# Kernel optimization log

Measured on AMD Instinct MI355X. Metric: run time of the kernel, lower is better.

The kernel has to match this reference:

```python
import jax, jax.numpy as jnp
import numpy as np

N = 50000        # nodes
E = 800000       # edges
IN_C = 128       # in_channels
HID = 256        # hidden_channels
HEADS = 4
HD = HID // HEADS
LAYERS = 4
GRAPHS = 64
OUT_C = 32
MAX_POS = 10
EPS = 1e-5


def layer_norm(x, g, b):
    mu = jnp.mean(x, axis=-1, keepdims=True)
    var = jnp.mean((x - mu) ** 2, axis=-1, keepdims=True)
    return (x - mu) / jnp.sqrt(var + EPS) * g + b


def setup_inputs() -> dict:
    key = jax.random.key(0)
    ks = jax.random.split(key, 32)
    s = 0.02
    inp = {
        "x": jax.random.normal(ks[0], (N, IN_C), dtype=jnp.float32),
        "edge_index": jax.random.randint(ks[1], (2, E), 0, N, dtype=jnp.int32),
        "pos_idx": jax.random.randint(ks[2], (N,), 0, MAX_POS, dtype=jnp.int32),
        "batch": jnp.sort(jax.random.randint(ks[3], (N,), 0, GRAPHS, dtype=jnp.int32)),
        # encoder MLP: Linear(IN->HID), ReLU, LN(HID), Linear(HID->HID); weights stored [in,out]
        "enc_w1": jax.random.normal(ks[4], (IN_C, HID)) * s,
        "enc_b1": jnp.zeros((HID,), jnp.float32),
        "enc_g": jnp.ones((HID,), jnp.float32),
        "enc_beta": jnp.zeros((HID,), jnp.float32),
        "enc_w2": jax.random.normal(ks[5], (HID, HID)) * s,
        "enc_b2": jnp.zeros((HID,), jnp.float32),
        "pos_emb": jax.random.normal(ks[6], (MAX_POS, HID)) * s,
        # stacked attention-layer params [LAYERS, ...]
        "Wq": jax.random.normal(ks[7], (LAYERS, HID, HID)) * s,
        "bq": jnp.zeros((LAYERS, HID), jnp.float32),
        "Wk": jax.random.normal(ks[8], (LAYERS, HID, HID)) * s,
        "bk": jnp.zeros((LAYERS, HID), jnp.float32),
        "Wv": jax.random.normal(ks[9], (LAYERS, HID, HID)) * s,
        "bv": jnp.zeros((LAYERS, HID), jnp.float32),
        "mlp_w1": jax.random.normal(ks[10], (LAYERS, 2 * HID, HID)) * s,
        "mlp_b1": jnp.zeros((LAYERS, HID), jnp.float32),
        "mlp_g": jnp.ones((LAYERS, HID), jnp.float32),
        "mlp_beta": jnp.zeros((LAYERS, HID), jnp.float32),
        "mlp_w2": jax.random.normal(ks[11], (LAYERS, HID, HID)) * s,
        "mlp_b2": jnp.zeros((LAYERS, HID), jnp.float32),
        # classifier
        "cls_w1": jax.random.normal(ks[12], (HID, HID)) * s,
        "cls_b1": jnp.zeros((HID,), jnp.float32),
        "cls_g": jnp.ones((HID,), jnp.float32),
        "cls_beta": jnp.zeros((HID,), jnp.float32),
        "cls_w2": jax.random.normal(ks[13], (HID, OUT_C)) * s,
        "cls_b2": jnp.zeros((OUT_C,), jnp.float32),
    }
    return inp


def reference(x, edge_index, pos_idx, batch,
              enc_w1, enc_b1, enc_g, enc_beta, enc_w2, enc_b2, pos_emb,
              Wq, bq, Wk, bk, Wv, bv,
              mlp_w1, mlp_b1, mlp_g, mlp_beta, mlp_w2, mlp_b2,
              cls_w1, cls_b1, cls_g, cls_beta, cls_w2, cls_b2):
    row, col = edge_index[0], edge_index[1]
    n = x.shape[0]
    e = row.shape[0]

    # NodeEncoder
    h = layer_norm(jax.nn.relu(x @ enc_w1 + enc_b1), enc_g, enc_beta) @ enc_w2 + enc_b2
    h = h + pos_emb[pos_idx]

    scale = jnp.asarray(HD, h.dtype) ** 0.5
    for l in range(LAYERS):
        Q = (h @ Wq[l] + bq[l]).reshape(n, HEADS, HD)
        K = (h @ Wk[l] + bk[l]).reshape(n, HEADS, HD)
        V = (h @ Wv[l] + bv[l]).reshape(n, HEADS, HD)
        # per-edge attention scores [E, HEADS]
        scores = jnp.sum(Q[row] * K[col], axis=-1) / scale
        # segment softmax over destination node `row`
        m = jax.ops.segment_max(scores, row, num_segments=n)
        ex = jnp.exp(scores - m[row])
        denom = jax.ops.segment_sum(ex, row, num_segments=n)
        w = ex / denom[row]                         # [E, HEADS]
        msg = (w[..., None] * V[col]).reshape(e, HID)
        agg = jax.ops.segment_sum(msg, row, num_segments=n)  # [N, HID]
        cat = jnp.concatenate([h, agg], axis=-1)
        z = layer_norm(jax.nn.relu(cat @ mlp_w1[l] + mlp_b1[l]), mlp_g[l], mlp_beta[l]) @ mlp_w2[l] + mlp_b2[l]
        h = z + h

    # global mean pool over graphs
    sums = jax.ops.segment_sum(h, batch, num_segments=GRAPHS)
    cnt = jax.ops.segment_sum(jnp.ones((n, 1), h.dtype), batch, num_segments=GRAPHS)
    pooled = sums / jnp.maximum(cnt, 1.0)

    out = layer_norm(jax.nn.relu(pooled @ cls_w1 + cls_b1), cls_g, cls_beta) @ cls_w2 + cls_b2
    return out
```

## Files before the change

kernel.cpp:

```cpp
#include <hip/hip_runtime.h>
#include <cstdint>

#define HID 256
#define HEADS 4
#define GRAPHS 64
#define OUTC 32
#define EPSV 1e-5f
#define PSPLIT 32

typedef __bf16 b16x8 __attribute__((ext_vector_type(8)));
typedef float  f32x4 __attribute__((ext_vector_type(4)));

__device__ __forceinline__ f32x4 mfma16(b16x8 a, b16x8 b, f32x4 c) {
    return __builtin_amdgcn_mfma_f32_16x16x32_bf16(a, b, c, 0, 0, 0);
}

__device__ __forceinline__ unsigned int pack_bf16(float a, float b) {
    unsigned short ua = __builtin_bit_cast(unsigned short, (__bf16)a);
    unsigned short ub = __builtin_bit_cast(unsigned short, (__bf16)b);
    return (unsigned int)ua | ((unsigned int)ub << 16);
}

__device__ __forceinline__ void unpack2(unsigned int u, float& lo, float& hi) {
    lo = __builtin_bit_cast(float, u << 16);
    hi = __builtin_bit_cast(float, u & 0xffff0000u);
}

__device__ __forceinline__ float b2f(unsigned short u) {
    return __builtin_bit_cast(float, (unsigned int)u << 16);
}

__device__ __forceinline__ void stage_gld128(char* buf, const unsigned short* __restrict__ src,
                                             int base, int tid)
{
#pragma unroll
    for (int i = 0; i < 16; i++) {
        int idx = i * 256 + tid;
        int r = idx >> 5;
        int u = idx & 31;
        int us = u ^ (r & 7);
        const void* gp = (const void*)(src + (size_t)(base + r) * HID + us * 8);
        __builtin_amdgcn_global_load_lds(
            (const __attribute__((address_space(1))) void*)gp,
            (__attribute__((address_space(3))) void*)(buf + idx * 16),
            16, 0, 0);
    }
}

__global__ __launch_bounds__(256) void wtrans_kernel(const float* __restrict__ W,
    unsigned short* __restrict__ Wt, int K, int C)
{
    __shared__ float tile[32][33];
    const float* Wm = W + (size_t)blockIdx.z * K * C;
    unsigned short* Wtm = Wt + (size_t)blockIdx.z * K * C;
    int k0 = blockIdx.x * 32, c0 = blockIdx.y * 32;
    int tx = threadIdx.x & 31, ty = threadIdx.x >> 5;
#pragma unroll
    for (int i = 0; i < 32; i += 8)
        tile[ty + i][tx] = Wm[(size_t)(k0 + ty + i) * C + c0 + tx];
    __syncthreads();
#pragma unroll
    for (int i = 0; i < 32; i += 8) {
        float v = tile[tx][ty + i];
        Wtm[(size_t)(c0 + ty + i) * K + k0 + tx] =
            __builtin_bit_cast(unsigned short, (__bf16)v);
    }
}

__global__ __launch_bounds__(256) void enc1_mfma(
    const float* __restrict__ in0, const unsigned short* __restrict__ Wt,
    const float* __restrict__ bias, const float* __restrict__ g,
    const float* __restrict__ be, unsigned short* __restrict__ outb, int n)
{
    constexpr int KTILE = 128, ROWB = 256;
    __shared__ __align__(16) char alds[64 * 256];
    __shared__ float red[4][64][2];
    int tid = threadIdx.x, lane = tid & 63, wv = tid >> 6;
    int cg = lane & 15, rg = lane >> 4;
    int base = blockIdx.x * 64;
    int cbase = wv * 64;

    f32x4 acc[4][4];
#pragma unroll
    for (int m = 0; m < 4; m++)
#pragma unroll
        for (int f = 0; f < 4; f++) acc[m][f] = (f32x4){0.f, 0.f, 0.f, 0.f};

#pragma unroll
    for (int i = 0; i < 8; i++) {
        int idx = (i * 256 + tid) * 4;
        int row = idx >> 7, k = idx & 127;
        int node = base + row;
        float4 v = {0.f, 0.f, 0.f, 0.f};
        if (node < n) v = *(const float4*)(in0 + (size_t)node * KTILE + k);
        uint2 pp; pp.x = pack_bf16(v.x, v.y); pp.y = pack_bf16(v.z, v.w);
        int off = row * ROWB + k * 2;
        off ^= (row & 7) << 4;
        *(uint2*)(alds + off) = pp;
    }
    __syncthreads();

#pragma unroll 2
    for (int k0 = 0; k0 < KTILE; k0 += 32) {
        b16x8 a[4], b[4];
#pragma unroll
        for (int m = 0; m < 4; m++) {
            int R = m * 16 + cg;
            int off = R * ROWB + (k0 + rg * 8) * 2;
            off ^= (R & 7) << 4;
            a[m] = __builtin_bit_cast(b16x8, *(const uint4*)(alds + off));
        }
#pragma unroll
        for (int f = 0; f < 4; f++) {
            const unsigned short* p = Wt + (size_t)(cbase + f * 16 + cg) * KTILE + k0 + rg * 8;
            b[f] = __builtin_bit_cast(b16x8, *(const uint4*)p);
        }
#pragma unroll
        for (int m = 0; m < 4; m++)
#pragma unroll
            for (int f = 0; f < 4; f++)
                acc[m][f] = mfma16(a[m], b[f], acc[m][f]);
    }

    float bias_v[4], g_v[4], be_v[4];
#pragma unroll
    for (int f = 0; f < 4; f++) {
        int col = cbase + f * 16 + cg;
        bias_v[f] = bias[col]; g_v[f] = g[col]; be_v[f] = be[col];
    }
#pragma unroll
    for (int m = 0; m < 4; m++)
#pragma unroll
        for (int f = 0; f < 4; f++)
#pragma unroll
            for (int r = 0; r < 4; r++)
                acc[m][f][r] = fmaxf(acc[m][f][r] + bias_v[f], 0.f);
#pragma unroll
    for (int m = 0; m < 4; m++)
#pragma unroll
        for (int r = 0; r < 4; r++) {
            float s = acc[m][0][r] + acc[m][1][r] + acc[m][2][r] + acc[m][3][r];
            float q = acc[m][0][r] * acc[m][0][r] + acc[m][1][r] * acc[m][1][r]
                    + acc[m][2][r] * acc[m][2][r] + acc[m][3][r] * acc[m][3][r];
#pragma unroll
            for (int o = 1; o < 16; o <<= 1) {
                s += __shfl_xor(s, o, 64); q += __shfl_xor(q, o, 64);
            }
            if (cg == 0) { int R = m * 16 + rg * 4 + r; red[wv][R][0] = s; red[wv][R][1] = q; }
        }
    __syncthreads();
#pragma unroll
    for (int m = 0; m < 4; m++)
#pragma unroll
        for (int r = 0; r < 4; r++) {
            int R = m * 16 + rg * 4 + r;
            float S = red[0][R][0] + red[1][R][0] + red[2][R][0] + red[3][R][0];
            float Q = red[0][R][1] + red[1][R][1] + red[2][R][1] + red[3][R][1];
            float mu = S * (1.f / HID);
            float rs = rsqrtf(Q * (1.f / HID) - mu * mu + EPSV);
            int row = base + R;
            if (row >= n) continue;
            size_t ro = (size_t)row * HID;
#pragma unroll
            for (int f = 0; f < 4; f++) {
                float v = (acc[m][f][r] - mu) * rs * g_v[f] + be_v[f];
                outb[ro + cbase + f * 16 + cg] = __builtin_bit_cast(unsigned short, (__bf16)v);
            }
        }
}

template<int NPASS, bool RELU_LN, bool ADD_RES, bool POS>
__global__ __launch_bounds__(256) void gemm128(
    const unsigned short* __restrict__ in0, const unsigned short* __restrict__ in1,
    const unsigned short* __restrict__ Wt, const float* __restrict__ bias,
    const float* __restrict__ g, const float* __restrict__ be,
    const unsigned short* __restrict__ addsrc, const float* __restrict__ pos_emb,
    const int* __restrict__ pidx, unsigned short* __restrict__ outb, int n)
{
    constexpr int KS = 256 * NPASS;
    __shared__ __align__(16) char alds[128 * 512];
    __shared__ float red[4][128][2];

    int tid = threadIdx.x, lane = tid & 63, wv = tid >> 6;
    int cg = lane & 15, rg = lane >> 4;
    int base = blockIdx.x * 128;
    int cbase = wv * 64;

    f32x4 acc[2][4][4];
#pragma unroll
    for (int t = 0; t < 2; t++)
#pragma unroll
        for (int m = 0; m < 4; m++)
#pragma unroll
            for (int f = 0; f < 4; f++) acc[t][m][f] = (f32x4){0.f, 0.f, 0.f, 0.f};

    for (int pass = 0; pass < NPASS; pass++) {
        if (pass) __syncthreads();
        const unsigned short* src = pass ? in1 : in0;
        const unsigned short* Wp = Wt + pass * 256;

        stage_gld128(alds, src, base, tid);
        __syncthreads();

#pragma unroll
        for (int kk = 0; kk < 8; kk++) {
            b16x8 b[4];
#pragma unroll
            for (int f = 0; f < 4; f++)
                b[f] = __builtin_bit_cast(b16x8, *(const uint4*)(
                    Wp + (size_t)(cbase + f * 16 + cg) * KS + kk * 32 + rg * 8));
#pragma unroll
            for (int t = 0; t < 2; t++) {
                b16x8 a[4];
#pragma unroll
                for (int m = 0; m < 4; m++) {
                    int R = t * 64 + m * 16 + cg;
                    int off = R * 512 + (kk * 32 + rg * 8) * 2;
                    off ^= (R & 7) << 4;
                    a[m] = __builtin_bit_cast(b16x8, *(const uint4*)(alds + off));
                }
#pragma unroll
                for (int m = 0; m < 4; m++)
#pragma unroll
                    for (int f = 0; f < 4; f++)
                        acc[t][m][f] = mfma16(a[m], b[f], acc[t][m][f]);
            }
        }
    }

    float bias_v[4], g_v[4], be_v[4];
#pragma unroll
    for (int f = 0; f < 4; f++) {
        int col = cbase + f * 16 + cg;
        bias_v[f] = bias[col];
        if (RELU_LN) { g_v[f] = g[col]; be_v[f] = be[col]; }
    }
#pragma unroll
    for (int t = 0; t < 2; t++)
#pragma unroll
        for (int m = 0; m < 4; m++)
#pragma unroll
            for (int f = 0; f < 4; f++)
#pragma unroll
                for (int r = 0; r < 4; r++) acc[t][m][f][r] += bias_v[f];

    if (RELU_LN) {
#pragma unroll
        for (int t = 0; t < 2; t++)
#pragma unroll
            for (int m = 0; m < 4; m++)
#pragma unroll
                for (int f = 0; f < 4; f++)
#pragma unroll
                    for (int r = 0; r < 4; r++)
                        acc[t][m][f][r] = fmaxf(acc[t][m][f][r], 0.f);
#pragma unroll
        for (int t = 0; t < 2; t++)
#pragma unroll
            for (int m = 0; m < 4; m++)
#pragma unroll
                for (int r = 0; r < 4; r++) {
                    float s = acc[t][m][0][r] + acc[t][m][1][r] + acc[t][m][2][r] + acc[t][m][3][r];
                    float q = acc[t][m][0][r] * acc[t][m][0][r] + acc[t][m][1][r] * acc[t][m][1][r]
                            + acc[t][m][2][r] * acc[t][m][2][r] + acc[t][m][3][r] * acc[t][m][3][r];
#pragma unroll
                    for (int o = 1; o < 16; o <<= 1) {
                        s += __shfl_xor(s, o, 64); q += __shfl_xor(q, o, 64);
                    }
                    if (cg == 0) {
                        int R = t * 64 + m * 16 + rg * 4 + r;
                        red[wv][R][0] = s; red[wv][R][1] = q;
                    }
                }
        __syncthreads();
#pragma unroll
        for (int t = 0; t < 2; t++)
#pragma unroll
            for (int m = 0; m < 4; m++)
#pragma unroll
                for (int r = 0; r < 4; r++) {
                    int R = t * 64 + m * 16 + rg * 4 + r;
                    float S = red[0][R][0] + red[1][R][0] + red[2][R][0] + red[3][R][0];
                    float Q = red[0][R][1] + red[1][R][1] + red[2][R][1] + red[3][R][1];
                    float mu = S * (1.f / HID);
                    float rs = rsqrtf(Q * (1.f / HID) - mu * mu + EPSV);
#pragma unroll
                    for (int f = 0; f < 4; f++)
                        acc[t][m][f][r] = (acc[t][m][f][r] - mu) * rs * g_v[f] + be_v[f];
                }
    }

#pragma unroll
    for (int t = 0; t < 2; t++)
#pragma unroll
        for (int m = 0; m < 4; m++)
#pragma unroll
            for (int r = 0; r < 4; r++) {
                int row = base + t * 64 + m * 16 + rg * 4 + r;
                if (row >= n) continue;
                size_t ro = (size_t)row * HID;
                int pid = 0;
                if (POS) pid = pidx[row];
#pragma unroll
                for (int f = 0; f < 4; f++) {
                    int col = cbase + f * 16 + cg;
                    float v = acc[t][m][f][r];
                    if (ADD_RES) v += b2f(addsrc[ro + col]);
                    if (POS)     v += pos_emb[(size_t)pid * HID + col];
                    outb[ro + col] = __builtin_bit_cast(unsigned short, (__bf16)v);
                }
            }
}

__global__ __launch_bounds__(256) void qkv128_kernel(
    const unsigned short* __restrict__ hsrc,
    const unsigned short* __restrict__ Wtq, const unsigned short* __restrict__ Wtk,
    const unsigned short* __restrict__ Wtv,
    const float* __restrict__ bq, const float* __restrict__ bk, const float* __restrict__ bv,
    unsigned short* __restrict__ Qo, unsigned short* __restrict__ Ko,
    unsigned short* __restrict__ Vo, int n)
{
    __shared__ __align__(16) char alds[128 * 512];
    int tid = threadIdx.x, lane = tid & 63, wv = tid >> 6;
    int cg = lane & 15, rg = lane >> 4;
    int base = blockIdx.x * 128;
    int cbase = wv * 64;

    stage_gld128(alds, hsrc, base, tid);
    __syncthreads();

    for (int mat = 0; mat < 3; mat++) {
        const unsigned short* Wp = (mat == 0) ? Wtq : (mat == 1) ? Wtk : Wtv;
        const float* bp = (mat == 0) ? bq : (mat == 1) ? bk : bv;
        unsigned short* op = (mat == 0) ? Qo : (mat == 1) ? Ko : Vo;

        f32x4 acc[2][4][4];
#pragma unroll
        for (int t = 0; t < 2; t++)
#pragma unroll
            for (int m = 0; m < 4; m++)
#pragma unroll
                for (int f = 0; f < 4; f++) acc[t][m][f] = (f32x4){0.f, 0.f, 0.f, 0.f};

#pragma unroll
        for (int kk = 0; kk < 8; kk++) {
            b16x8 b[4];
#pragma unroll
            for (int f = 0; f < 4; f++)
                b[f] = __builtin_bit_cast(b16x8, *(const uint4*)(
                    Wp + (size_t)(cbase + f * 16 + cg) * 256 + kk * 32 + rg * 8));
#pragma unroll
            for (int t = 0; t < 2; t++) {
                b16x8 a[4];
#pragma unroll
                for (int m = 0; m < 4; m++) {
                    int R = t * 64 + m * 16 + cg;
                    int off = R * 512 + (kk * 32 + rg * 8) * 2;
                    off ^= (R & 7) << 4;
                    a[m] = __builtin_bit_cast(b16x8, *(const uint4*)(alds + off));
                }
#pragma unroll
                for (int m = 0; m < 4; m++)
#pragma unroll
                    for (int f = 0; f < 4; f++)
                        acc[t][m][f] = mfma16(a[m], b[f], acc[t][m][f]);
            }
        }

        float bias_v[4];
#pragma unroll
        for (int f = 0; f < 4; f++) bias_v[f] = bp[cbase + f * 16 + cg];
#pragma unroll
        for (int t = 0; t < 2; t++)
#pragma unroll
            for (int m = 0; m < 4; m++)
#pragma unroll
                for (int r = 0; r < 4; r++) {
                    int row = base + t * 64 + m * 16 + rg * 4 + r;
                    if (row >= n) continue;
                    size_t ro = (size_t)row * HID;
#pragma unroll
                    for (int f = 0; f < 4; f++) {
                        float v = acc[t][m][f][r] + bias_v[f];
                        op[ro + cbase + f * 16 + cg] =
                            __builtin_bit_cast(unsigned short, (__bf16)v);
                    }
                }
    }
}

__global__ void count_kernel(const int* __restrict__ row, int* __restrict__ counts, int e)
{
    int i = blockIdx.x * blockDim.x + threadIdx.x;
    if (i < e) atomicAdd(&counts[row[i]], 1);
}

__global__ __launch_bounds__(256) void scan1_kernel(const int* __restrict__ counts,
    int* __restrict__ offs, int* __restrict__ bsum, int n)
{
    __shared__ int wsumS[4];
    int tid = threadIdx.x, b = blockIdx.x;
    int i = b * 256 + tid;
    int v = (i < n) ? counts[i] : 0;
    int lane = tid & 63, wv = tid >> 6;
    int s = v;
#pragma unroll
    for (int o = 1; o < 64; o <<= 1) { int t = __shfl_up(s, o, 64); if (lane >= o) s += t; }
    if (lane == 63) wsumS[wv] = s;
    __syncthreads();
    int add = 0;
    for (int j = 0; j < wv; j++) add += wsumS[j];
    s += add;
    if (i < n) offs[i + 1] = s;
    if (tid == 255) bsum[b] = s;
}

__global__ __launch_bounds__(256) void scan2_kernel(int* __restrict__ bsum, int nb)
{
    __shared__ int wsumS[4];
    int tid = threadIdx.x;
    int v = (tid < nb) ? bsum[tid] : 0;
    int lane = tid & 63, wv = tid >> 6;
    int s = v;
#pragma unroll
    for (int o = 1; o < 64; o <<= 1) { int t = __shfl_up(s, o, 64); if (lane >= o) s += t; }
    if (lane == 63) wsumS[wv] = s;
    __syncthreads();
    int add = 0;
    for (int j = 0; j < wv; j++) add += wsumS[j];
    s += add;
    if (tid < nb) bsum[tid] = s;
}

__global__ __launch_bounds__(256) void scan3_kernel(int* __restrict__ offs,
    const int* __restrict__ bsum, int n)
{
    int tid = threadIdx.x, b = blockIdx.x;
    int i = b * 256 + tid;
    if (i == 0) offs[0] = 0;
    if (i < n && b > 0) offs[i + 1] += bsum[b - 1];
}

__global__ void scatter_kernel(const int* __restrict__ row, const int* __restrict__ col,
    const int* __restrict__ offs, int* __restrict__ cur, int* __restrict__ ccol, int e)
{
    int i = blockIdx.x * blockDim.x + threadIdx.x;
    if (i >= e) return;
    int r = row[i];
    int pos = atomicAdd(&cur[r], 1);
    ccol[offs[r] + pos] = col[i];
}

__global__ __launch_bounds__(256) void attn_hw_kernel(
    const unsigned short* __restrict__ Qm, const unsigned short* __restrict__ Km,
    const unsigned short* __restrict__ Vm,
    const int* __restrict__ offs, const int* __restrict__ ccol,
    unsigned short* __restrict__ agg, int n)
{
    int tid = threadIdx.x;
    int hw = tid >> 5;
    int l32 = tid & 31;
    int node = blockIdx.x * 8 + hw;
    if (node >= n) return;
    int start = offs[node], fin = offs[node + 1];
    size_t rowoff = (size_t)node * HID + l32 * 8;
    if (start == fin) {
        uint4 z = {0u, 0u, 0u, 0u};
        *(uint4*)(agg + rowoff) = z;
        return;
    }

    uint4 qr = *(const uint4*)(Qm + rowoff);
    float qf[8];
    unpack2(qr.x, qf[0], qf[1]);
    unpack2(qr.y, qf[2], qf[3]);
    unpack2(qr.z, qf[4], qf[5]);
    unpack2(qr.w, qf[6], qf[7]);

    float m = -3.0e38f, d = 0.f;
    float acc[8];
#pragma unroll
    for (int j = 0; j < 8; j++) acc[j] = 0.f;

    for (int i = start; i < fin; i++) {
        int c = ccol[i];
        const unsigned short* kp = Km + (size_t)c * HID + l32 * 8;
        const unsigned short* vp = Vm + (size_t)c * HID + l32 * 8;
        uint4 kr = *(const uint4*)kp;
        uint4 vr = *(const uint4*)vp;
        float k0, k1, k2, k3, k4, k5, k6, k7;
        unpack2(kr.x, k0, k1); unpack2(kr.y, k2, k3);
        unpack2(kr.z, k4, k5); unpack2(kr.w, k6, k7);
        float p = qf[0] * k0 + qf[1] * k1 + qf[2] * k2 + qf[3] * k3
                + qf[4] * k4 + qf[5] * k5 + qf[6] * k6 + qf[7] * k7;
        p += __shfl_xor(p, 1, 64);
        p += __shfl_xor(p, 2, 64);
        p += __shfl_xor(p, 4, 64);
        float s = p * 0.125f;
        float mn = fmaxf(m, s);
        float sc = __expf(m - mn);
        float w = __expf(s - mn);
        d = d * sc + w;
        float v0, v1, v2, v3, v4, v5, v6, v7;
        unpack2(vr.x, v0, v1); unpack2(vr.y, v2, v3);
        unpack2(vr.z, v4, v5); unpack2(vr.w, v6, v7);
        acc[0] = acc[0] * sc + w * v0;  acc[1] = acc[1] * sc + w * v1;
        acc[2] = acc[2] * sc + w * v2;  acc[3] = acc[3] * sc + w * v3;
        acc[4] = acc[4] * sc + w * v4;  acc[5] = acc[5] * sc + w * v5;
        acc[6] = acc[6] * sc + w * v6;  acc[7] = acc[7] * sc + w * v7;
        m = mn;
    }

    float inv = 1.f / d;
    uint4 out;
    out.x = pack_bf16(acc[0] * inv, acc[1] * inv);
    out.y = pack_bf16(acc[2] * inv, acc[3] * inv);
    out.z = pack_bf16(acc[4] * inv, acc[5] * inv);
    out.w = pack_bf16(acc[6] * inv, acc[7] * inv);
    *(uint4*)(agg + rowoff) = out;
}

__global__ void bounds_kernel(const int* __restrict__ batch, int* __restrict__ gb, int n)
{
    int g = threadIdx.x;
    if (g > GRAPHS) return;
    int lo = 0, hi = n;
    while (lo < hi) { int mid = (lo + hi) >> 1; if (batch[mid] < g) lo = mid + 1; else hi = mid; }
    gb[g] = lo;
}

__global__ __launch_bounds__(256) void pool_partial_kernel(
    const unsigned short* __restrict__ h16,
    const int* __restrict__ gb, float* __restrict__ partial)
{
    int s = blockIdx.x, g = blockIdx.y, tid = threadIdx.x;
    int lo = gb[g], hi = gb[g + 1];
    float sum = 0.f;
    for (int i = lo + s; i < hi; i += PSPLIT)
        sum += b2f(h16[(size_t)i * HID + tid]);
    partial[((size_t)g * PSPLIT + s) * HID + tid] = sum;
}

__global__ __launch_bounds__(256) void pool_reduce_kernel(const float* __restrict__ partial,
    const int* __restrict__ gb, float* __restrict__ pooled)
{
    int g = blockIdx.x, tid = threadIdx.x;
    float sum = 0.f;
#pragma unroll
    for (int s = 0; s < PSPLIT; s++) sum += partial[((size_t)g * PSPLIT + s) * HID + tid];
    int cnt = gb[g + 1] - gb[g];
    pooled[g * HID + tid] = sum / fmaxf((float)cnt, 1.f);
}

__global__ __launch_bounds__(256) void cls_kernel(const float* __restrict__ pooled,
    const float* __restrict__ W1, const float* __restrict__ b1,
    const float* __restrict__ g, const float* __restrict__ be,
    const float* __restrict__ W2, const float* __restrict__ b2,
    float* __restrict__ out)
{
    __shared__ float pin[HID];
    __shared__ float hbuf[HID];
    __shared__ float red2[4][2];
    int tid = threadIdx.x, gi = blockIdx.x;
    int lane = tid & 63, wv = tid >> 6;
    pin[tid] = pooled[gi * HID + tid];
    __syncthreads();
    float acc = 0.f;
    for (int k = 0; k < HID; k++) acc += pin[k] * W1[k * HID + tid];
    acc = fmaxf(acc + b1[tid], 0.f);
    float s = acc, q = acc * acc;
#pragma unroll
    for (int o = 1; o < 64; o <<= 1) { s += __shfl_xor(s, o, 64); q += __shfl_xor(q, o, 64); }
    if (lane == 0) { red2[wv][0] = s; red2[wv][1] = q; }
    __syncthreads();
    float S = red2[0][0] + red2[1][0] + red2[2][0] + red2[3][0];
    float Q = red2[0][1] + red2[1][1] + red2[2][1] + red2[3][1];
    float mu = S * (1.f / HID);
    float rs = rsqrtf(Q * (1.f / HID) - mu * mu + EPSV);
    hbuf[tid] = (acc - mu) * rs * g[tid] + be[tid];
    __syncthreads();
    if (tid < OUTC) {
        float o = 0.f;
        for (int k = 0; k < HID; k++) o += hbuf[k] * W2[k * OUTC + tid];
        out[gi * OUTC + tid] = o + b2[tid];
    }
}

extern "C" void kernel_launch(void* const* d_in, const int* in_sizes, int n_in,
                              void* d_out, int out_size, void* d_ws, size_t ws_size,
                              hipStream_t stream)
{
    const float* x        = (const float*)d_in[0];
    const int*   ei       = (const int*)d_in[1];
    const int*   pidx     = (const int*)d_in[2];
    const int*   batch    = (const int*)d_in[3];
    const float* enc_w1   = (const float*)d_in[4];
    const float* enc_b1   = (const float*)d_in[5];
    const float* enc_g    = (const float*)d_in[6];
    const float* enc_beta = (const float*)d_in[7];
    const float* enc_w2   = (const float*)d_in[8];
    const float* enc_b2   = (const float*)d_in[9];
    const float* pos_emb  = (const float*)d_in[10];
    const float* Wq       = (const float*)d_in[11];
    const float* bq       = (const float*)d_in[12];
    const float* Wk       = (const float*)d_in[13];
    const float* bk       = (const float*)d_in[14];
    const float* Wv       = (const float*)d_in[15];
    const float* bv       = (const float*)d_in[16];
    const float* mlp_w1   = (const float*)d_in[17];
    const float* mlp_b1   = (const float*)d_in[18];
    const float* mlp_g    = (const float*)d_in[19];
    const float* mlp_beta = (const float*)d_in[20];
    const float* mlp_w2   = (const float*)d_in[21];
    const float* mlp_b2   = (const float*)d_in[22];
    const float* cls_w1   = (const float*)d_in[23];
    const float* cls_b1   = (const float*)d_in[24];
    const float* cls_g    = (const float*)d_in[25];
    const float* cls_beta = (const float*)d_in[26];
    const float* cls_w2   = (const float*)d_in[27];
    const float* cls_b2   = (const float*)d_in[28];

    int n = in_sizes[2];
    int e = in_sizes[1] / 2;
    const int* row = ei;
    const int* col = ei + e;

    char* p = (char*)d_ws;
    auto alloc = [&](size_t bytes) -> void* {
        void* r = (void*)p;
        p += (bytes + 255) & ~(size_t)255;
        return r;
    };
    size_t NH = (size_t)n * HID;
    unsigned short* h16  = (unsigned short*)alloc(NH * 2);
    unsigned short* a16  = (unsigned short*)alloc(NH * 2);
    unsigned short* m16  = (unsigned short*)alloc(NH * 2);
    unsigned short* Qb   = (unsigned short*)alloc(NH * 2);
    unsigned short* Kb   = (unsigned short*)alloc(NH * 2);
    unsigned short* Vb   = (unsigned short*)alloc(NH * 2);
    float* partial = (float*)alloc((size_t)GRAPHS * PSPLIT * HID * 4);
    float* pooled  = (float*)alloc((size_t)GRAPHS * HID * 4);
    int* counts = (int*)alloc((size_t)n * 4);
    int* offs   = (int*)alloc((size_t)(n + 1) * 4);
    int* cur    = (int*)alloc((size_t)n * 4);
    int* ccol   = (int*)alloc((size_t)e * 4);
    int* bsum   = (int*)alloc(1024);
    int* gb     = (int*)alloc((GRAPHS + 1) * 4);
    unsigned short* wt_e1 = (unsigned short*)alloc((size_t)128 * 256 * 2);
    unsigned short* wt_e2 = (unsigned short*)alloc((size_t)256 * 256 * 2);
    unsigned short* wt_q  = (unsigned short*)alloc((size_t)4 * 256 * 256 * 2);
    unsigned short* wt_k  = (unsigned short*)alloc((size_t)4 * 256 * 256 * 2);
    unsigned short* wt_v  = (unsigned short*)alloc((size_t)4 * 256 * 256 * 2);
    unsigned short* wt_m1 = (unsigned short*)alloc((size_t)4 * 512 * 256 * 2);
    unsigned short* wt_m2 = (unsigned short*)alloc((size_t)4 * 256 * 256 * 2);

    int gblocks64  = (n + 63) / 64;
    int gblocks128 = (n + 127) / 128;
    int nb = (n + 255) / 256;

    wtrans_kernel<<<dim3(4, 8, 1),  256, 0, stream>>>(enc_w1, wt_e1, 128, 256);
    wtrans_kernel<<<dim3(8, 8, 1),  256, 0, stream>>>(enc_w2, wt_e2, 256, 256);
    wtrans_kernel<<<dim3(8, 8, 4),  256, 0, stream>>>(Wq,     wt_q,  256, 256);
    wtrans_kernel<<<dim3(8, 8, 4),  256, 0, stream>>>(Wk,     wt_k,  256, 256);
    wtrans_kernel<<<dim3(8, 8, 4),  256, 0, stream>>>(Wv,     wt_v,  256, 256);
    wtrans_kernel<<<dim3(16, 8, 4), 256, 0, stream>>>(mlp_w1, wt_m1, 512, 256);
    wtrans_kernel<<<dim3(8, 8, 4),  256, 0, stream>>>(mlp_w2, wt_m2, 256, 256);

    hipMemsetAsync(counts, 0, (size_t)n * 4, stream);
    hipMemsetAsync(cur, 0, (size_t)n * 4, stream);
    count_kernel<<<(e + 255) / 256, 256, 0, stream>>>(row, counts, e);
    scan1_kernel<<<nb, 256, 0, stream>>>(counts, offs, bsum, n);
    scan2_kernel<<<1, 256, 0, stream>>>(bsum, nb);
    scan3_kernel<<<nb, 256, 0, stream>>>(offs, bsum, n);
    scatter_kernel<<<(e + 255) / 256, 256, 0, stream>>>(row, col, offs, cur, ccol, e);
    bounds_kernel<<<1, 128, 0, stream>>>(batch, gb, n);

    enc1_mfma<<<gblocks64, 256, 0, stream>>>(x, wt_e1, enc_b1, enc_g, enc_beta, m16, n);
    gemm128<1, false, false, true><<<gblocks128, 256, 0, stream>>>(
        m16, nullptr, wt_e2, enc_b2, nullptr, nullptr, nullptr, pos_emb, pidx, h16, n);

    int ablocks = (n + 7) / 8;
    for (int l = 0; l < 4; l++) {
        size_t wo = (size_t)l * 256 * 256;
        size_t bo = (size_t)l * HID;
        qkv128_kernel<<<gblocks128, 256, 0, stream>>>(
            h16, wt_q + wo, wt_k + wo, wt_v + wo, bq + bo, bk + bo, bv + bo,
            Qb, Kb, Vb, n);
        attn_hw_kernel<<<ablocks, 256, 0, stream>>>(Qb, Kb, Vb, offs, ccol, a16, n);
        gemm128<2, true, false, false><<<gblocks128, 256, 0, stream>>>(
            h16, a16, wt_m1 + (size_t)l * 512 * 256, mlp_b1 + bo,
            mlp_g + bo, mlp_beta + bo, nullptr, nullptr, nullptr, m16, n);
        gemm128<1, false, true, false><<<gblocks128, 256, 0, stream>>>(
            m16, nullptr, wt_m2 + wo, mlp_b2 + bo, nullptr, nullptr, h16, nullptr, nullptr,
            h16, n);
    }

    pool_partial_kernel<<<dim3(PSPLIT, GRAPHS), 256, 0, stream>>>(h16, gb, partial);
    pool_reduce_kernel<<<GRAPHS, 256, 0, stream>>>(partial, gb, pooled);
    cls_kernel<<<GRAPHS, 256, 0, stream>>>(pooled, cls_w1, cls_b1, cls_g, cls_beta,
                                           cls_w2, cls_b2, (float*)d_out);
}
```

Measured before the change: 1.241 ms.

## Fuse MLP GEMMs with layernorm in one kernel and prefetch attention K/V rows

Merges the two per-layer MLP GEMMs into one kernel. The ReLU+LayerNorm intermediate stays in LDS as bf16 and feeds the second GEMM directly, so the m16 round trip to global memory and one launch per layer go away. Separately, the attention edge loop now software-pipelines K/V gathers two edges ahead to hide latency. The cost is higher register pressure, which may lower occupancy, and the residual is now read and written in place in h16.

```diff
diff --git a/kernel.cpp b/kernel.cpp
--- a/kernel.cpp
+++ b/kernel.cpp
@@ -308,6 +308,181 @@
                     if (ADD_RES) v += b2f(addsrc[ro + col]);
                     if (POS)     v += pos_emb[(size_t)pid * HID + col];
                     outb[ro + col] = __builtin_bit_cast(unsigned short, (__bf16)v);
+                }
+            }
+}
+
+__global__ __launch_bounds__(256) void mlp_fused(
+    const unsigned short* __restrict__ h16, const unsigned short* __restrict__ a16,
+    const unsigned short* __restrict__ Wt1, const float* __restrict__ b1,
+    const float* __restrict__ g, const float* __restrict__ be,
+    const unsigned short* __restrict__ Wt2, const float* __restrict__ b2,
+    unsigned short* __restrict__ hout, int n)
+{
+    __shared__ __align__(16) char alds[128 * 512];
+    __shared__ float red[4][128][2];
+    int tid = threadIdx.x, lane = tid & 63, wv = tid >> 6;
+    int cg = lane & 15, rg = lane >> 4;
+    int base = blockIdx.x * 128;
+    int cbase = wv * 64;
+
+    f32x4 acc[2][4][4];
+#pragma unroll
+    for (int t = 0; t < 2; t++)
+#pragma unroll
+        for (int m = 0; m < 4; m++)
+#pragma unroll
+            for (int f = 0; f < 4; f++) acc[t][m][f] = (f32x4){0.f, 0.f, 0.f, 0.f};
+
+    for (int pass = 0; pass < 2; pass++) {
+        if (pass) __syncthreads();
+        const unsigned short* src = pass ? a16 : h16;
+        const unsigned short* Wp = Wt1 + pass * 256;
+        stage_gld128(alds, src, base, tid);
+        __syncthreads();
+#pragma unroll
+        for (int kk = 0; kk < 8; kk++) {
+            b16x8 b[4];
+#pragma unroll
+            for (int f = 0; f < 4; f++)
+                b[f] = __builtin_bit_cast(b16x8, *(const uint4*)(
+                    Wp + (size_t)(cbase + f * 16 + cg) * 512 + kk * 32 + rg * 8));
+#pragma unroll
+            for (int t = 0; t < 2; t++) {
+                b16x8 a[4];
+#pragma unroll
+                for (int m = 0; m < 4; m++) {
+                    int R = t * 64 + m * 16 + cg;
+                    int off = R * 512 + (kk * 32 + rg * 8) * 2;
+                    off ^= (R & 7) << 4;
+                    a[m] = __builtin_bit_cast(b16x8, *(const uint4*)(alds + off));
+                }
+#pragma unroll
+                for (int m = 0; m < 4; m++)
+#pragma unroll
+                    for (int f = 0; f < 4; f++)
+                        acc[t][m][f] = mfma16(a[m], b[f], acc[t][m][f]);
+            }
+        }
+    }
+
+    float b1_v[4], g_v[4], be_v[4];
+#pragma unroll
+    for (int f = 0; f < 4; f++) {
+        int col = cbase + f * 16 + cg;
+        b1_v[f] = b1[col]; g_v[f] = g[col]; be_v[f] = be[col];
+    }
+#pragma unroll
+    for (int t = 0; t < 2; t++)
+#pragma unroll
+        for (int m = 0; m < 4; m++)
+#pragma unroll
+            for (int f = 0; f < 4; f++)
+#pragma unroll
+                for (int r = 0; r < 4; r++)
+                    acc[t][m][f][r] = fmaxf(acc[t][m][f][r] + b1_v[f], 0.f);
+#pragma unroll
+    for (int t = 0; t < 2; t++)
+#pragma unroll
+        for (int m = 0; m < 4; m++)
+#pragma unroll
+            for (int r = 0; r < 4; r++) {
+                float s = acc[t][m][0][r] + acc[t][m][1][r] + acc[t][m][2][r] + acc[t][m][3][r];
+                float q = acc[t][m][0][r] * acc[t][m][0][r] + acc[t][m][1][r] * acc[t][m][1][r]
+                        + acc[t][m][2][r] * acc[t][m][2][r] + acc[t][m][3][r] * acc[t][m][3][r];
+#pragma unroll
+                for (int o = 1; o < 16; o <<= 1) {
+                    s += __shfl_xor(s, o, 64); q += __shfl_xor(q, o, 64);
+                }
+                if (cg == 0) {
+                    int R = t * 64 + m * 16 + rg * 4 + r;
+                    red[wv][R][0] = s; red[wv][R][1] = q;
+                }
+            }
+    __syncthreads();
+#pragma unroll
+    for (int t = 0; t < 2; t++)
+#pragma unroll
+        for (int m = 0; m < 4; m++)
+#pragma unroll
+            for (int r = 0; r < 4; r++) {
+                int R = t * 64 + m * 16 + rg * 4 + r;
+                float S = red[0][R][0] + red[1][R][0] + red[2][R][0] + red[3][R][0];
+                float Q = red[0][R][1] + red[1][R][1] + red[2][R][1] + red[3][R][1];
+                float mu = S * (1.f / HID);
+                float rs = rsqrtf(Q * (1.f / HID) - mu * mu + EPSV);
+#pragma unroll
+                for (int f = 0; f < 4; f++)
+                    acc[t][m][f][r] = (acc[t][m][f][r] - mu) * rs * g_v[f] + be_v[f];
+            }
+
+    __syncthreads();
+#pragma unroll
+    for (int t = 0; t < 2; t++)
+#pragma unroll
+        for (int m = 0; m < 4; m++)
+#pragma unroll
+            for (int r = 0; r < 4; r++) {
+                int R = t * 64 + m * 16 + rg * 4 + r;
+#pragma unroll
+                for (int f = 0; f < 4; f++) {
+                    int col = cbase + f * 16 + cg;
+                    int off = R * 512 + col * 2;
+                    off ^= (R & 7) << 4;
+                    *(unsigned short*)(alds + off) =
+                        __builtin_bit_cast(unsigned short, (__bf16)acc[t][m][f][r]);
+                }
+            }
+    __syncthreads();
+
+#pragma unroll
+    for (int t = 0; t < 2; t++)
+#pragma unroll
+        for (int m = 0; m < 4; m++)
+#pragma unroll
+            for (int f = 0; f < 4; f++) acc[t][m][f] = (f32x4){0.f, 0.f, 0.f, 0.f};
+#pragma unroll
+    for (int kk = 0; kk < 8; kk++) {
+        b16x8 b[4];
+#pragma unroll
+        for (int f = 0; f < 4; f++)
+            b[f] = __builtin_bit_cast(b16x8, *(const uint4*)(
+                Wt2 + (size_t)(cbase + f * 16 + cg) * 256 + kk * 32 + rg * 8));
+#pragma unroll
+        for (int t = 0; t < 2; t++) {
+            b16x8 a[4];
+#pragma unroll
+            for (int m = 0; m < 4; m++) {
+                int R = t * 64 + m * 16 + cg;
+                int off = R * 512 + (kk * 32 + rg * 8) * 2;
+                off ^= (R & 7) << 4;
+                a[m] = __builtin_bit_cast(b16x8, *(const uint4*)(alds + off));
+            }
+#pragma unroll
+            for (int m = 0; m < 4; m++)
+#pragma unroll
+                for (int f = 0; f < 4; f++)
+                    acc[t][m][f] = mfma16(a[m], b[f], acc[t][m][f]);
+        }
+    }
+
+    float b2_v[4];
+#pragma unroll
+    for (int f = 0; f < 4; f++) b2_v[f] = b2[cbase + f * 16 + cg];
+#pragma unroll
+    for (int t = 0; t < 2; t++)
+#pragma unroll
+        for (int m = 0; m < 4; m++)
+#pragma unroll
+            for (int r = 0; r < 4; r++) {
+                int row = base + t * 64 + m * 16 + rg * 4 + r;
+                if (row >= n) continue;
+                size_t ro = (size_t)row * HID;
+#pragma unroll
+                for (int f = 0; f < 4; f++) {
+                    int col = cbase + f * 16 + cg;
+                    float v = acc[t][m][f][r] + b2_v[f] + b2f(hout[ro + col]);
+                    hout[ro + col] = __builtin_bit_cast(unsigned short, (__bf16)v);
                 }
             }
 }
@@ -482,12 +657,22 @@
 #pragma unroll
     for (int j = 0; j < 8; j++) acc[j] = 0.f;
 
+    int c0 = ccol[start];
+    int c1 = (start + 1 < fin) ? ccol[start + 1] : c0;
+    uint4 krA = *(const uint4*)(Km + (size_t)c0 * HID + l32 * 8);
+    uint4 vrA = *(const uint4*)(Vm + (size_t)c0 * HID + l32 * 8);
+    uint4 krB = *(const uint4*)(Km + (size_t)c1 * HID + l32 * 8);
+    uint4 vrB = *(const uint4*)(Vm + (size_t)c1 * HID + l32 * 8);
+
     for (int i = start; i < fin; i++) {
-        int c = ccol[i];
-        const unsigned short* kp = Km + (size_t)c * HID + l32 * 8;
-        const unsigned short* vp = Vm + (size_t)c * HID + l32 * 8;
-        uint4 kr = *(const uint4*)kp;
-        uint4 vr = *(const uint4*)vp;
+        uint4 kr = krA, vr = vrA;
+        krA = krB; vrA = vrB;
+        int ip = i + 2;
+        if (ip < fin) {
+            int c = ccol[ip];
+            krB = *(const uint4*)(Km + (size_t)c * HID + l32 * 8);
+            vrB = *(const uint4*)(Vm + (size_t)c * HID + l32 * 8);
+        }
         float k0, k1, k2, k3, k4, k5, k6, k7;
         unpack2(kr.x, k0, k1); unpack2(kr.y, k2, k3);
         unpack2(kr.z, k4, k5); unpack2(kr.w, k6, k7);
@@ -687,12 +872,9 @@
             h16, wt_q + wo, wt_k + wo, wt_v + wo, bq + bo, bk + bo, bv + bo,
             Qb, Kb, Vb, n);
         attn_hw_kernel<<<ablocks, 256, 0, stream>>>(Qb, Kb, Vb, offs, ccol, a16, n);
-        gemm128<2, true, false, false><<<gblocks128, 256, 0, stream>>>(
+        mlp_fused<<<gblocks128, 256, 0, stream>>>(
             h16, a16, wt_m1 + (size_t)l * 512 * 256, mlp_b1 + bo,
-            mlp_g + bo, mlp_beta + bo, nullptr, nullptr, nullptr, m16, n);
-        gemm128<1, false, true, false><<<gblocks128, 256, 0, stream>>>(
-            m16, nullptr, wt_m2 + wo, mlp_b2 + bo, nullptr, nullptr, h16, nullptr, nullptr,
-            h16, n);
+            mlp_g + bo, mlp_beta + bo, wt_m2 + wo, mlp_b2 + bo, h16, n);
     }
 
     pool_partial_kernel<<<dim3(PSPLIT, GRAPHS), 256, 0, stream>>>(h16, gb, partial);
```

After: 1.249 ms. About the same (+0.6%).
